# Optimization experiments

Measured on AMD Instinct MI355X. Metric: run time of the kernel, lower is better.

The kernel has to match this reference:

```python
import jax, jax.numpy as jnp
import numpy as np

B, S, D = 2, 2048, 1024
H, DH, DL, DR = 16, 64, 512, 64
DHID, N_SHARED, N_ROUTED, TOPK = 512, 2, 8, 2
EPS = 1e-6


def setup_inputs() -> dict:
    key = jax.random.key(0)
    ks = jax.random.split(key, 16)
    w = lambda k, shp: jax.random.normal(k, shp, dtype=jnp.float32) * 0.02
    return {
        "x": jax.random.normal(ks[0], (B, S, D), dtype=jnp.float32),
        "mask": jnp.tril(jnp.ones((S, S), dtype=bool)),  # causal
        "w_q": w(ks[1], (D, H * (DH + DR))),
        "w_dkv": w(ks[2], (D, DL)),
        "w_uk": w(ks[3], (DL, H * DH)),
        "w_uv": w(ks[4], (DL, H * DH)),
        "w_kr": w(ks[5], (D, DR)),
        "w_o": w(ks[6], (H * DH, D)),
        "attn_norm_w": jnp.ones((D,), jnp.float32),
        "mlp_norm_w": jnp.ones((D,), jnp.float32),
        "gate_w": w(ks[7], (D, N_ROUTED)),
        "wr_gate": w(ks[8], (N_ROUTED, D, DHID)),
        "wr_up": w(ks[9], (N_ROUTED, D, DHID)),
        "wr_down": w(ks[10], (N_ROUTED, DHID, D)),
        "ws_gate": w(ks[11], (N_SHARED, D, DHID)),
        "ws_up": w(ks[12], (N_SHARED, D, DHID)),
        "ws_down": w(ks[13], (N_SHARED, DHID, D)),
    }


def _rmsnorm(x, w):
    x32 = x.astype(jnp.float32)
    n = x32 * jax.lax.rsqrt(jnp.mean(x32 * x32, axis=-1, keepdims=True) + EPS)
    return n.astype(x.dtype) * w


def _rope_tables(seq_len, dim):
    half = dim // 2
    inv = 1.0 / (10000.0 ** (jnp.arange(half, dtype=jnp.float32) / half))
    ang = jnp.arange(seq_len, dtype=jnp.float32)[:, None] * inv[None, :]  # [S, dim/2]
    return jnp.cos(ang), jnp.sin(ang)


def _rope(t, cos, sin):
    # t: [..., S, dim]; rotate-half convention
    t1, t2 = jnp.split(t, 2, axis=-1)
    return jnp.concatenate([t1 * cos - t2 * sin, t2 * cos + t1 * sin], axis=-1)


def _layer(x, mask, w_q, w_dkv, w_uk, w_uv, w_kr, w_o, attn_norm_w, mlp_norm_w,
           gate_w, wr_gate, wr_up, wr_down, ws_gate, ws_up, ws_down):
    # ---- pre-norm MLA attention + residual ----
    h = _rmsnorm(x, attn_norm_w)
    cos, sin = _rope_tables(S, DR)

    q = (h @ w_q).reshape(B, S, H, DH + DR).transpose(0, 2, 1, 3)  # [B,H,S,DH+DR]
    q_c, q_r = q[..., :DH], _rope(q[..., DH:], cos, sin)

    latent = h @ w_dkv                                              # [B,S,DL]
    k_c = (latent @ w_uk).reshape(B, S, H, DH).transpose(0, 2, 1, 3)  # [B,H,S,DH]
    v = (latent @ w_uv).reshape(B, S, H, DH).transpose(0, 2, 1, 3)
    k_r = _rope(h @ w_kr, cos, sin)                                 # [B,S,DR] shared across heads

    scale = 1.0 / np.sqrt(DH + DR)
    scores = (jnp.einsum("bhqd,bhkd->bhqk", q_c, k_c)
              + jnp.einsum("bhqd,bkd->bhqk", q_r, k_r)) * scale
    scores = jnp.where(mask, scores, jnp.float32(-1e9))
    attn = jax.nn.softmax(scores, axis=-1)
    ctx = jnp.einsum("bhqk,bhkd->bhqd", attn, v)                    # [B,H,S,DH]
    attn_out = ctx.transpose(0, 2, 1, 3).reshape(B, S, H * DH) @ w_o
    x = x + attn_out

    # ---- pre-norm shared + routed MoE FFN + residual ----
    h = _rmsnorm(x, mlp_norm_w).reshape(-1, D)                      # [T,D]
    probs = jax.nn.softmax(h @ gate_w, axis=-1)                     # [T,NR]
    vals, idx = jax.lax.top_k(probs, TOPK)                          # [T,K]
    gw = vals / jnp.sum(vals, axis=-1, keepdims=True)
    dense_w = jnp.sum(jax.nn.one_hot(idx, N_ROUTED, dtype=h.dtype) * gw[..., None], axis=1)  # [T,NR]

    g = jax.nn.silu(jnp.einsum("td,edh->teh", h, wr_gate))
    u = jnp.einsum("td,edh->teh", h, wr_up)
    y = jnp.einsum("teh,ehd->ted", g * u, wr_down)                  # [T,NR,D]
    routed = jnp.einsum("ted,te->td", y, dense_w)

    gs = jax.nn.silu(jnp.einsum("td,sdh->tsh", h, ws_gate))
    us = jnp.einsum("td,sdh->tsh", h, ws_up)
    shared = jnp.einsum("tsh,shd->td", gs * us, ws_down)

    return x + (routed + shared).reshape(B, S, D)


def reference(x, mask, w_q, w_dkv, w_uk, w_uv, w_kr, w_o, attn_norm_w, mlp_norm_w,
              gate_w, wr_gate, wr_up, wr_down, ws_gate, ws_up, ws_down):
    return _layer(x, mask, w_q, w_dkv, w_uk, w_uv, w_kr, w_o, attn_norm_w, mlp_norm_w,
                  gate_w, wr_gate, wr_up, wr_down, ws_gate, ws_up, ws_down)
```

## Files before the change

### kernel.cpp

```cpp
#include <hip/hip_runtime.h>
#include <hip/hip_bf16.h>
#include <stdint.h>

typedef unsigned short u16;
typedef __attribute__((ext_vector_type(8))) short short8;
typedef __attribute__((ext_vector_type(4))) float f32x4;
typedef __attribute__((ext_vector_type(4))) int i32x4;
typedef __attribute__((ext_vector_type(2))) unsigned int u32x2;

#define B_    2
#define S_    2048
#define D_    1024
#define H_    16
#define T_    (B_*S_)

static __device__ __forceinline__ float b2f(u16 h) { return __uint_as_float(((uint32_t)h) << 16); }
static __device__ __forceinline__ u16 f2b(float f) {
    uint32_t u = __float_as_uint(f);
    u += 0x7fffu + ((u >> 16) & 1u);
    return (u16)(u >> 16);
}
static __device__ __forceinline__ uint32_t pack2(float a, float b) {
    return (uint32_t)f2b(a) | ((uint32_t)f2b(b) << 16);
}
static __device__ __forceinline__ uint32_t cvtpk(float a, float b) {
    uint32_t r;
    asm("v_cvt_pk_bf16_f32 %0, %1, %2" : "=v"(r) : "v"(a), "v"(b));
    return r;
}
#define MFMA(a,b,c) __builtin_amdgcn_mfma_f32_16x16x32_bf16(a,b,c,0,0,0)

static __device__ __forceinline__ void gl2lds16(const void* g, void* l) {
    __builtin_amdgcn_global_load_lds((const __attribute__((address_space(1))) void*)g,
                                     (__attribute__((address_space(3))) void*)l, 16, 0, 0);
}

__global__ __launch_bounds__(256) void transpose_cvt(const float* __restrict__ in,
    u16* __restrict__ out, int K, int N, long inEZ, long outEZ)
{
    __shared__ float tile[32][33];
    const int e = blockIdx.z;
    const float* ip = in + (long)e * inEZ;
    u16* op = out + (long)e * outEZ;
    int n0 = blockIdx.x * 32, k0 = blockIdx.y * 32;
    int tx = threadIdx.x, ty = threadIdx.y;
#pragma unroll
    for (int i = 0; i < 4; ++i) {
        int k = k0 + ty + 8 * i, n = n0 + tx;
        tile[ty + 8 * i][tx] = (k < K && n < N) ? ip[(long)k * N + n] : 0.f;
    }
    __syncthreads();
#pragma unroll
    for (int i = 0; i < 4; ++i) {
        int n = n0 + ty + 8 * i, k = k0 + tx;
        if (n < N && k < K) op[(long)n * K + k] = f2b(tile[tx][ty + 8 * i]);
    }
}

__global__ __launch_bounds__(256) void gemm_k(const u16* __restrict__ A, long lda,
    const u16* __restrict__ Bt, long ldb, void* __restrict__ Cv, long ldc, int K,
    int mode, const float* __restrict__ resid)
{
    __shared__ u16 As[128 * 32];
    __shared__ u16 Bs[128 * 32];
    const int tid = threadIdx.x, lane = tid & 63, wave = tid >> 6;
    const int wm = (wave & 1) * 64, wn = (wave >> 1) * 64;
    const int quad = lane >> 4, rr = lane & 15, q8 = quad * 8;
    const long row0 = (long)blockIdx.y * 128, col0 = (long)blockIdx.x * 128;
    f32x4 acc[4][4];
#pragma unroll
    for (int i = 0; i < 4; ++i)
#pragma unroll
        for (int j = 0; j < 4; ++j)
#pragma unroll
            for (int c = 0; c < 4; ++c) acc[i][j][c] = 0.f;
    const int band = wave * 32;
    const u16* ga = A + (row0 + band + (lane >> 2)) * lda + (lane & 3) * 8;
    const u16* gb = Bt + (col0 + band + (lane >> 2)) * ldb + (lane & 3) * 8;
    u16* la = &As[band * 32];
    u16* lb = &Bs[band * 32];
    for (int k0 = 0; k0 < K; k0 += 32) {
        gl2lds16(ga + k0, la);
        gl2lds16(ga + k0 + 16 * lda, la + 16 * 32);
        gl2lds16(gb + k0, lb);
        gl2lds16(gb + k0 + 16 * ldb, lb + 16 * 32);
        __syncthreads();
        short8 af[4], bf[4];
#pragma unroll
        for (int mi = 0; mi < 4; ++mi) af[mi] = *(const short8*)&As[(wm + mi * 16 + rr) * 32 + q8];
#pragma unroll
        for (int ni = 0; ni < 4; ++ni) bf[ni] = *(const short8*)&Bs[(wn + ni * 16 + rr) * 32 + q8];
#pragma unroll
        for (int mi = 0; mi < 4; ++mi)
#pragma unroll
            for (int ni = 0; ni < 4; ++ni)
                acc[mi][ni] = MFMA(af[mi], bf[ni], acc[mi][ni]);
        __syncthreads();
    }
#pragma unroll
    for (int mi = 0; mi < 4; ++mi)
#pragma unroll
        for (int ni = 0; ni < 4; ++ni)
#pragma unroll
            for (int rg = 0; rg < 4; ++rg) {
                long r = row0 + wm + mi * 16 + quad * 4 + rg;
                long c = col0 + wn + ni * 16 + rr;
                float v = acc[mi][ni][rg];
                if (mode == 1)      ((u16*)Cv)[r * ldc + c] = f2b(v);
                else if (mode == 2) ((float*)Cv)[r * ldc + c] += v;
                else                ((float*)Cv)[r * ldc + c] = v + resid[r * 1024 + c];
            }
}

__global__ __launch_bounds__(256) void gemm_shdown(const u16* __restrict__ A,
    const u16* __restrict__ BtBase, float* __restrict__ Cv)
{
    __shared__ u16 As[128 * 32];
    __shared__ u16 Bs[128 * 32];
    const int tid = threadIdx.x, lane = tid & 63, wave = tid >> 6;
    const int wm = (wave & 1) * 64, wn = (wave >> 1) * 64;
    const int quad = lane >> 4, rr = lane & 15, q8 = quad * 8;
    const long row0 = (long)blockIdx.y * 128, col0 = (long)blockIdx.x * 128;
    f32x4 acc[4][4];
#pragma unroll
    for (int i = 0; i < 4; ++i)
#pragma unroll
        for (int j = 0; j < 4; ++j)
#pragma unroll
            for (int c = 0; c < 4; ++c) acc[i][j][c] = 0.f;
    const int band = wave * 32;
    const long arow = row0 + band + (lane >> 2);
    const long brow = col0 + band + (lane >> 2);
    u16* la = &As[band * 32];
    u16* lb = &Bs[band * 32];
    for (int k0 = 0; k0 < 1024; k0 += 32) {
        const long aoff = (k0 < 512) ? (long)k0 : (long)(512 + k0);
        const long boff = (k0 < 512) ? (long)k0 : (long)(524288 - 512 + k0);
        const u16* ga = A + arow * 2048 + aoff + (lane & 3) * 8;
        const u16* gb = BtBase + brow * 512 + boff + (lane & 3) * 8;
        gl2lds16(ga, la);
        gl2lds16(ga + 16 * 2048, la + 16 * 32);
        gl2lds16(gb, lb);
        gl2lds16(gb + 16 * 512, lb + 16 * 32);
        __syncthreads();
        short8 af[4], bf[4];
#pragma unroll
        for (int mi = 0; mi < 4; ++mi) af[mi] = *(const short8*)&As[(wm + mi * 16 + rr) * 32 + q8];
#pragma unroll
        for (int ni = 0; ni < 4; ++ni) bf[ni] = *(const short8*)&Bs[(wn + ni * 16 + rr) * 32 + q8];
#pragma unroll
        for (int mi = 0; mi < 4; ++mi)
#pragma unroll
            for (int ni = 0; ni < 4; ++ni)
                acc[mi][ni] = MFMA(af[mi], bf[ni], acc[mi][ni]);
        __syncthreads();
    }
#pragma unroll
    for (int mi = 0; mi < 4; ++mi)
#pragma unroll
        for (int ni = 0; ni < 4; ++ni)
#pragma unroll
            for (int rg = 0; rg < 4; ++rg) {
                long r = row0 + wm + mi * 16 + quad * 4 + rg;
                long c = col0 + wn + ni * 16 + rr;
                Cv[r * 1024 + c] += acc[mi][ni][rg];
            }
}

__global__ __launch_bounds__(256) void gemm_gather(const u16* __restrict__ H2,
    const u16* __restrict__ BtAll, u16* __restrict__ C,
    const int* __restrict__ cnt, const int* __restrict__ off,
    const int* __restrict__ elist)
{
    const int e = blockIdx.z;
    const int cntE = cnt[e], offE = off[e];
    const int m0 = blockIdx.y * 128;
    if (m0 >= cntE) return;
    const u16* Bt = BtAll + (long)e * 1024 * 1024;
    __shared__ u16 As[128 * 32];
    __shared__ u16 Bs[128 * 32];
    const int tid = threadIdx.x, lane = tid & 63, wave = tid >> 6;
    const int wm = (wave & 1) * 64, wn = (wave >> 1) * 64;
    const int quad = lane >> 4, rr = lane & 15, q8 = quad * 8;
    const long col0 = (long)blockIdx.x * 128;
    f32x4 acc[4][4];
#pragma unroll
    for (int i = 0; i < 4; ++i)
#pragma unroll
        for (int j = 0; j < 4; ++j)
#pragma unroll
            for (int c = 0; c < 4; ++c) acc[i][j][c] = 0.f;
    const int band = wave * 32;
    int r0 = m0 + band + (lane >> 2);
    int r1 = r0 + 16;
    int tok0 = elist[offE + (r0 < cntE ? r0 : cntE - 1)];
    int tok1 = elist[offE + (r1 < cntE ? r1 : cntE - 1)];
    const u16* ga0 = H2 + (long)tok0 * 1024 + (lane & 3) * 8;
    const u16* ga1 = H2 + (long)tok1 * 1024 + (lane & 3) * 8;
    const u16* gb = Bt + (col0 + band + (lane >> 2)) * 1024L + (lane & 3) * 8;
    u16* la = &As[band * 32];
    u16* lb = &Bs[band * 32];
    for (int k0 = 0; k0 < 1024; k0 += 32) {
        gl2lds16(ga0 + k0, la);
        gl2lds16(ga1 + k0, la + 16 * 32);
        gl2lds16(gb + k0, lb);
        gl2lds16(gb + k0 + 16 * 1024, lb + 16 * 32);
        __syncthreads();
        short8 af[4], bf[4];
#pragma unroll
        for (int mi = 0; mi < 4; ++mi) af[mi] = *(const short8*)&As[(wm + mi * 16 + rr) * 32 + q8];
#pragma unroll
        for (int ni = 0; ni < 4; ++ni) bf[ni] = *(const short8*)&Bs[(wn + ni * 16 + rr) * 32 + q8];
#pragma unroll
        for (int mi = 0; mi < 4; ++mi)
#pragma unroll
            for (int ni = 0; ni < 4; ++ni)
                acc[mi][ni] = MFMA(af[mi], bf[ni], acc[mi][ni]);
        __syncthreads();
    }
#pragma unroll
    for (int mi = 0; mi < 4; ++mi)
#pragma unroll
        for (int ni = 0; ni < 4; ++ni)
#pragma unroll
            for (int rg = 0; rg < 4; ++rg) {
                int ml = wm + mi * 16 + quad * 4 + rg;
                long c = col0 + wn + ni * 16 + rr;
                if (m0 + ml < cntE)
                    C[(long)(offE + m0 + ml) * 1024 + c] = f2b(acc[mi][ni][rg]);
            }
}

__global__ __launch_bounds__(256) void gemm_slot(const u16* __restrict__ Act,
    const u16* __restrict__ BtAll, u16* __restrict__ rout,
    const int* __restrict__ cnt, const int* __restrict__ off)
{
    const int e = blockIdx.z;
    const int cntE = cnt[e], offE = off[e];
    const int m0 = blockIdx.y * 128;
    if (m0 >= cntE) return;
    const u16* Bt = BtAll + (long)e * 1024 * 512;
    __shared__ u16 As[128 * 32];
    __shared__ u16 Bs[128 * 32];
    const int tid = threadIdx.x, lane = tid & 63, wave = tid >> 6;
    const int wm = (wave & 1) * 64, wn = (wave >> 1) * 64;
    const int quad = lane >> 4, rr = lane & 15, q8 = quad * 8;
    const long col0 = (long)blockIdx.x * 128;
    f32x4 acc[4][4];
#pragma unroll
    for (int i = 0; i < 4; ++i)
#pragma unroll
        for (int j = 0; j < 4; ++j)
#pragma unroll
            for (int c = 0; c < 4; ++c) acc[i][j][c] = 0.f;
    const int band = wave * 32;
    int r0 = offE + m0 + band + (lane >> 2); if (r0 > 8191) r0 = 8191;
    int r1 = r0 + 16; if (r1 > 8191) r1 = 8191;
    const u16* ga0 = Act + (long)r0 * 1024 + (lane & 3) * 8;
    const u16* ga1 = Act + (long)r1 * 1024 + (lane & 3) * 8;
    const u16* gb = Bt + (col0 + band + (lane >> 2)) * 512L + (lane & 3) * 8;
    u16* la = &As[band * 32];
    u16* lb = &Bs[band * 32];
    for (int k0 = 0; k0 < 512; k0 += 32) {
        gl2lds16(ga0 + k0, la);
        gl2lds16(ga1 + k0, la + 16 * 32);
        gl2lds16(gb + k0, lb);
        gl2lds16(gb + k0 + 16 * 512, lb + 16 * 32);
        __syncthreads();
        short8 af[4], bf[4];
#pragma unroll
        for (int mi = 0; mi < 4; ++mi) af[mi] = *(const short8*)&As[(wm + mi * 16 + rr) * 32 + q8];
#pragma unroll
        for (int ni = 0; ni < 4; ++ni) bf[ni] = *(const short8*)&Bs[(wn + ni * 16 + rr) * 32 + q8];
#pragma unroll
        for (int mi = 0; mi < 4; ++mi)
#pragma unroll
            for (int ni = 0; ni < 4; ++ni)
                acc[mi][ni] = MFMA(af[mi], bf[ni], acc[mi][ni]);
        __syncthreads();
    }
#pragma unroll
    for (int mi = 0; mi < 4; ++mi)
#pragma unroll
        for (int ni = 0; ni < 4; ++ni)
#pragma unroll
            for (int rg = 0; rg < 4; ++rg) {
                int ml = wm + mi * 16 + quad * 4 + rg;
                long c = col0 + wn + ni * 16 + rr;
                if (m0 + ml < cntE)
                    rout[(long)(offE + m0 + ml) * 1024 + c] = f2b(acc[mi][ni][rg]);
            }
}

__global__ __launch_bounds__(256) void rmsnorm_wave(const float* __restrict__ x,
    const float* __restrict__ w, u16* __restrict__ out)
{
    const int t = blockIdx.x * 4 + (threadIdx.x >> 6);
    const int lane = threadIdx.x & 63;
    const float* xp = x + (size_t)t * D_;
    f32x4 v[4];
    float s = 0.f;
#pragma unroll
    for (int i = 0; i < 4; ++i) {
        v[i] = *(const f32x4*)&xp[lane * 4 + i * 256];
#pragma unroll
        for (int j = 0; j < 4; ++j) s += v[i][j] * v[i][j];
    }
#pragma unroll
    for (int o = 32; o > 0; o >>= 1) s += __shfl_xor(s, o);
    const float inv = rsqrtf(s * (1.f / D_) + 1e-6f);
    u16* op = out + (size_t)t * D_;
#pragma unroll
    for (int i = 0; i < 4; ++i) {
        const int d = lane * 4 + i * 256;
        f32x4 wv = *(const f32x4*)&w[d];
        u32x2 pk;
        pk[0] = pack2(v[i][0] * inv * wv[0], v[i][1] * inv * wv[1]);
        pk[1] = pack2(v[i][2] * inv * wv[2], v[i][3] * inv * wv[3]);
        *(u32x2*)&op[d] = pk;
    }
}

__global__ __launch_bounds__(256) void rmsnorm_gate_fused(const float* __restrict__ xm,
    const float* __restrict__ nw, const float* __restrict__ gw, u16* __restrict__ h2,
    int* __restrict__ tok_e, float* __restrict__ tok_w)
{
    const int t = blockIdx.x * 4 + (threadIdx.x >> 6);
    const int lane = threadIdx.x & 63;
    const float* xp = xm + (size_t)t * D_;
    f32x4 v[4];
    float s = 0.f;
#pragma unroll
    for (int i = 0; i < 4; ++i) {
        v[i] = *(const f32x4*)&xp[lane * 4 + i * 256];
#pragma unroll
        for (int j = 0; j < 4; ++j) s += v[i][j] * v[i][j];
    }
#pragma unroll
    for (int o = 32; o > 0; o >>= 1) s += __shfl_xor(s, o);
    const float inv = rsqrtf(s * (1.f / D_) + 1e-6f);
    u16* op = h2 + (size_t)t * D_;
    float part[8] = {0,0,0,0,0,0,0,0};
#pragma unroll
    for (int i = 0; i < 4; ++i) {
        const int d = lane * 4 + i * 256;
        f32x4 wv = *(const f32x4*)&nw[d];
        float hv[4];
#pragma unroll
        for (int j = 0; j < 4; ++j) hv[j] = v[i][j] * inv * wv[j];
        u32x2 pk;
        pk[0] = pack2(hv[0], hv[1]);
        pk[1] = pack2(hv[2], hv[3]);
        *(u32x2*)&op[d] = pk;
#pragma unroll
        for (int j = 0; j < 4; ++j) {
            const float* gp = gw + (size_t)(d + j) * 8;
#pragma unroll
            for (int e = 0; e < 8; ++e) part[e] += hv[j] * gp[e];
        }
    }
#pragma unroll
    for (int e = 0; e < 8; ++e)
#pragma unroll
        for (int o = 32; o > 0; o >>= 1) part[e] += __shfl_xor(part[e], o);
    if (lane == 0) {
        float mx = part[0];
#pragma unroll
        for (int e = 1; e < 8; ++e) mx = fmaxf(mx, part[e]);
        float p[8];
#pragma unroll
        for (int e = 0; e < 8; ++e) p[e] = __expf(part[e] - mx);
        int i0 = 0;
#pragma unroll
        for (int e = 1; e < 8; ++e) if (p[e] > p[i0]) i0 = e;
        int i1 = (i0 == 0) ? 1 : 0;
#pragma unroll
        for (int e = 0; e < 8; ++e) { if (e == i0) continue; if (p[e] > p[i1]) i1 = e; }
        float sw = p[i0] + p[i1];
        tok_e[2 * t] = i0;  tok_e[2 * t + 1] = i1;
        tok_w[2 * t] = p[i0] / sw;  tok_w[2 * t + 1] = p[i1] / sw;
    }
}

__global__ __launch_bounds__(256) void moe_route(const int* __restrict__ tok_e,
    int* __restrict__ cnt, int* __restrict__ off,
    int* __restrict__ elist, int* __restrict__ tslot)
{
    const int E = blockIdx.x;
    const int tid = threadIdx.x, lane = tid & 63, wave = tid >> 6;
    int ev[32];
#pragma unroll
    for (int i = 0; i < 8; ++i)
        *(i32x4*)&ev[i * 4] = *(const i32x4*)&tok_e[tid * 32 + i * 4];
    int c8[8] = {0,0,0,0,0,0,0,0};
#pragma unroll
    for (int k = 0; k < 32; ++k) ++c8[ev[k] & 7];
    int incl[8];
#pragma unroll
    for (int e = 0; e < 8; ++e) {
        int vv = c8[e];
#pragma unroll
        for (int d = 1; d < 64; d <<= 1) {
            int tmp = __shfl_up(vv, d);
            if (lane >= d) vv += tmp;
        }
        incl[e] = vv;
    }
    __shared__ int wtot[4][8];
    if (lane == 63)
#pragma unroll
        for (int e = 0; e < 8; ++e) wtot[wave][e] = incl[e];
    __syncthreads();
    int tot[8];
#pragma unroll
    for (int e = 0; e < 8; ++e) tot[e] = wtot[0][e] + wtot[1][e] + wtot[2][e] + wtot[3][e];
    int waveoff = 0;
    for (int w = 0; w < 4; ++w) if (w < wave) waveoff += wtot[w][E];
    int offE = 0;
#pragma unroll
    for (int e = 0; e < 8; ++e) if (e < E) offE += tot[e];
    int rank = offE + waveoff + (incl[E] - c8[E]);
#pragma unroll
    for (int k = 0; k < 32; ++k) {
        if ((ev[k] & 7) == E) {
            int p = tid * 32 + k;
            elist[rank] = p >> 1;
            tslot[p] = rank;
            ++rank;
        }
    }
    if (tid == 0) { cnt[E] = tot[E]; off[E] = offE; }
}

__global__ __launch_bounds__(256) void rope_all(u16* __restrict__ proj)
{
    int idx = blockIdx.x * 256 + threadIdx.x;
    int i = idx & 31;
    int r = idx >> 5;
    int t = r / 17, which = r - t * 17;
    int s = t & (S_ - 1);
    float inv = __expf(-(float)i * 0.28782313662425575f);
    float ang = (float)s * inv;
    float c = cosf(ang), sn = sinf(ang);
    u16* base = proj + (size_t)t * 2688 + (which < 16 ? which * 128 + 64 : 2560);
    float t1 = b2f(base[i]), t2 = b2f(base[32 + i]);
    base[i]      = f2b(t1 * c - t2 * sn);
    base[32 + i] = f2b(t2 * c + t1 * sn);
}

#define KS  136
#define PS2 72
__global__ __launch_bounds__(256, 4) void attn_flash(const u16* __restrict__ proj,
    const u16* __restrict__ kc, const u16* __restrict__ vt, u16* __restrict__ ctx)
{
    const int qidx = blockIdx.x >> 5;
    const int qt = (qidx < 16) ? (31 - qidx) : (qidx - 16);
    const int bh = blockIdx.x & 31;
    const int b = bh >> 4, h = bh & 15;
    const int q0 = qt * 64;
    const int tid = threadIdx.x, lane = tid & 63, wave = tid >> 6;
    const int quad = lane >> 4, rr = lane & 15, q8 = quad * 8;
    const int wm2 = wave * 16;

    __shared__ u16 Ks[64 * KS];
    __shared__ u16 Ps[64 * PS2];

    const long tbase = (long)b * S_ + q0;
    short8 qf[4];
#pragma unroll
    for (int d0 = 0; d0 < 4; ++d0)
        qf[d0] = *(const short8*)&proj[(tbase + wm2 + rr) * 2688 + h * 128 + d0 * 32 + q8];

    f32x4 accO[4];
    float m_i = -3e38f, l_i = 0.f;
#pragma unroll
    for (int vi = 0; vi < 4; ++vi)
#pragma unroll
        for (int rg = 0; rg < 4; ++rg) accO[vi][rg] = 0.f;
    const float sc = 0.08838834764831845f * 1.4426950408889634f;

    const int srow0 = tid >> 3, scc0 = (tid & 7) * 8;
    const u16* kcp = kc   + ((long)b * S_ + srow0) * 1024 + h * 64 + scc0;
    const u16* krp = proj + ((long)b * S_ + srow0) * 2688 + 2560 + scc0;
    const u16* vbase = vt + (size_t)(h * 64 + rr) * 4096 + b * 2048 + q8;

    const int nkt = qt + 1;
    short8 rk0 = *(const short8*)(kcp);
    short8 rk1 = *(const short8*)(kcp + 32 * 1024);
    short8 rm0 = *(const short8*)(krp);
    short8 rm1 = *(const short8*)(krp + (size_t)32 * 2688);

    for (int kt = 0; kt < nkt; ++kt) {
        const int k0 = kt * 64;
        *(short8*)&Ks[srow0 * KS + scc0]        = rk0;
        *(short8*)&Ks[(srow0 + 32) * KS + scc0] = rk1;
        *(short8*)&Ks[srow0 * KS + 64 + scc0]        = rm0;
        *(short8*)&Ks[(srow0 + 32) * KS + 64 + scc0] = rm1;
        __syncthreads();

        const size_t k0s = (kt + 1 < nkt) ? (size_t)(k0 + 64) : 0;
        short8 nk0 = *(const short8*)(kcp + k0s * 1024);
        short8 nk1 = *(const short8*)(kcp + k0s * 1024 + 32 * 1024);
        short8 nm0 = *(const short8*)(krp + k0s * 2688);
        short8 nm1 = *(const short8*)(krp + k0s * 2688 + (size_t)32 * 2688);

        f32x4 accS[4];
#pragma unroll
        for (int ki = 0; ki < 4; ++ki)
#pragma unroll
            for (int rg = 0; rg < 4; ++rg) accS[ki][rg] = 0.f;
        __builtin_amdgcn_s_setprio(1);
#pragma unroll
        for (int d0 = 0; d0 < 4; ++d0) {
            short8 kf[4];
#pragma unroll
            for (int ki = 0; ki < 4; ++ki) kf[ki] = *(const short8*)&Ks[(ki * 16 + rr) * KS + d0 * 32 + q8];
#pragma unroll
            for (int ki = 0; ki < 4; ++ki) accS[ki] = MFMA(kf[ki], qf[d0], accS[ki]);
        }
        __builtin_amdgcn_s_setprio(0);
        __syncthreads();

        short8 vf0[4], vf1[4];
#pragma unroll
        for (int vi = 0; vi < 4; ++vi) {
            vf0[vi] = *(const short8*)(vbase + (size_t)vi * 16 * 4096 + k0);
            vf1[vi] = *(const short8*)(vbase + (size_t)vi * 16 * 4096 + k0 + 32);
        }

        float mx = -3e38f;
        if (kt == qt) {
            const int qg = q0 + wm2 + rr;
#pragma unroll
            for (int ki = 0; ki < 4; ++ki)
#pragma unroll
                for (int rg = 0; rg < 4; ++rg) {
                    float w = accS[ki][rg] * sc;
                    if (k0 + ki * 16 + quad * 4 + rg > qg) w = -1e30f;
                    accS[ki][rg] = w;
                    mx = fmaxf(mx, w);
                }
        } else {
#pragma unroll
            for (int ki = 0; ki < 4; ++ki)
#pragma unroll
                for (int rg = 0; rg < 4; ++rg) {
                    float w = accS[ki][rg] * sc;
                    accS[ki][rg] = w;
                    mx = fmaxf(mx, w);
                }
        }
        mx = fmaxf(mx, __shfl_xor(mx, 16));
        mx = fmaxf(mx, __shfl_xor(mx, 32));
        if (__any(mx > m_i)) {
            float mnew = fmaxf(m_i, mx);
            float alpha = exp2f(m_i - mnew);
            m_i = mnew;
            l_i *= alpha;
#pragma unroll
            for (int vi = 0; vi < 4; ++vi)
#pragma unroll
                for (int rg = 0; rg < 4; ++rg) accO[vi][rg] *= alpha;
        }
        float ps = 0.f;
#pragma unroll
        for (int ki = 0; ki < 4; ++ki) {
            float p0 = exp2f(accS[ki][0] - m_i);
            float p1 = exp2f(accS[ki][1] - m_i);
            float p2 = exp2f(accS[ki][2] - m_i);
            float p3 = exp2f(accS[ki][3] - m_i);
            ps += (p0 + p1) + (p2 + p3);
            u32x2 pk; pk[0] = cvtpk(p0, p1); pk[1] = cvtpk(p2, p3);
            *(u32x2*)&Ps[(wm2 + rr) * PS2 + ki * 16 + quad * 4] = pk;
        }
        ps += __shfl_xor(ps, 16);
        ps += __shfl_xor(ps, 32);
        l_i += ps;

        short8 pf0 = *(const short8*)&Ps[(wm2 + rr) * PS2 + q8];
        short8 pf1 = *(const short8*)&Ps[(wm2 + rr) * PS2 + 32 + q8];
        __builtin_amdgcn_s_setprio(1);
#pragma unroll
        for (int vi = 0; vi < 4; ++vi) accO[vi] = MFMA(vf0[vi], pf0, accO[vi]);
#pragma unroll
        for (int vi = 0; vi < 4; ++vi) accO[vi] = MFMA(vf1[vi], pf1, accO[vi]);
        __builtin_amdgcn_s_setprio(0);

        rk0 = nk0; rk1 = nk1; rm0 = nm0; rm1 = nm1;
    }
    {
        float linv = 1.f / l_i;
        long t = tbase + wm2 + rr;
#pragma unroll
        for (int vi = 0; vi < 4; ++vi) {
            u32x2 pk;
            pk[0] = pack2(accO[vi][0] * linv, accO[vi][1] * linv);
            pk[1] = pack2(accO[vi][2] * linv, accO[vi][3] * linv);
            *(u32x2*)&ctx[t * 1024 + h * 64 + vi * 16 + quad * 4] = pk;
        }
    }
}

__global__ __launch_bounds__(256) void silu_mul(u16* __restrict__ gu, int nPairRows)
{
    int i = blockIdx.x * 256 + threadIdx.x;
    if (i >= nPairRows * 64) return;
    int row = i >> 6, j8 = (i & 63) * 8;
    long base = (long)row * 1024;
    short8 g8 = *(const short8*)&gu[base + j8];
    short8 u8 = *(const short8*)&gu[base + 512 + j8];
    short8 r;
#pragma unroll
    for (int j = 0; j < 8; ++j) {
        float g = b2f((u16)g8[j]), u = b2f((u16)u8[j]);
        r[j] = (short)f2b(g / (1.f + __expf(-g)) * u);
    }
    *(short8*)&gu[base + j8] = r;
}

__global__ __launch_bounds__(256) void final_kernel(const float* __restrict__ xm,
    const u16* __restrict__ rout, const int* __restrict__ tok_slot,
    const float* __restrict__ tok_w, float* __restrict__ out)
{
    long i = ((long)blockIdx.x * 256 + threadIdx.x) * 4;
    int t = (int)(i >> 10), d = (int)(i & 1023);
    int s0 = tok_slot[2 * t], s1 = tok_slot[2 * t + 1];
    float w0 = tok_w[2 * t], w1 = tok_w[2 * t + 1];
    f32x4 xv = *(const f32x4*)&xm[i];
    u32x2 r0 = *(const u32x2*)&rout[(long)s0 * 1024 + d];
    u32x2 r1 = *(const u32x2*)&rout[(long)s1 * 1024 + d];
    f32x4 o;
    o[0] = xv[0] + w0 * b2f((u16)(r0[0] & 0xffffu)) + w1 * b2f((u16)(r1[0] & 0xffffu));
    o[1] = xv[1] + w0 * b2f((u16)(r0[0] >> 16))     + w1 * b2f((u16)(r1[0] >> 16));
    o[2] = xv[2] + w0 * b2f((u16)(r0[1] & 0xffffu)) + w1 * b2f((u16)(r1[1] & 0xffffu));
    o[3] = xv[3] + w0 * b2f((u16)(r0[1] >> 16))     + w1 * b2f((u16)(r1[1] >> 16));
    *(f32x4*)&out[i] = o;
}

#define OFF_XMID   0UL
#define OFF_H      16777216UL
#define OFF_PROJ   25165824UL
#define OFF_WGU    25165824UL
#define OFF_KC     47185920UL
#define OFF_WD     47185920UL
#define OFF_VT     55574528UL
#define OFF_GUR    57671680UL
#define OFF_CTX    63963136UL
#define OFF_WATT   72351744UL
#define OFF_ROUT   74448896UL
#define OFF_GUS    91226112UL
#define OFF_TOKE   108003328UL
#define OFF_TOKW   108036096UL
#define OFF_TSLOT  108068864UL
#define OFF_ELIST  108101632UL
#define OFF_META   108134400UL

extern "C" void kernel_launch(void* const* d_in, const int* in_sizes, int n_in,
                              void* d_out, int out_size, void* d_ws, size_t ws_size,
                              hipStream_t stream)
{
    const float* x       = (const float*)d_in[0];
    const float* w_q     = (const float*)d_in[2];
    const float* w_dkv   = (const float*)d_in[3];
    const float* w_uk    = (const float*)d_in[4];
    const float* w_uv    = (const float*)d_in[5];
    const float* w_kr    = (const float*)d_in[6];
    const float* w_o     = (const float*)d_in[7];
    const float* attn_nw = (const float*)d_in[8];
    const float* mlp_nw  = (const float*)d_in[9];
    const float* gate_w  = (const float*)d_in[10];
    const float* wr_gate = (const float*)d_in[11];
    const float* wr_up   = (const float*)d_in[12];
    const float* wr_down = (const float*)d_in[13];
    const float* ws_gate = (const float*)d_in[14];
    const float* ws_up   = (const float*)d_in[15];
    const float* ws_down = (const float*)d_in[16];
    float* out = (float*)d_out;

    char* W = (char*)d_ws;
    float* x_mid = (float*)(W + OFF_XMID);
    u16* h      = (u16*)(W + OFF_H);
    u16* h2     = (u16*)(W + OFF_H);
    u16* proj   = (u16*)(W + OFF_PROJ);
    u16* wgu_t  = (u16*)(W + OFF_WGU);
    u16* kc     = (u16*)(W + OFF_KC);
    u16* wd_t   = (u16*)(W + OFF_WD);
    u16* vt     = (u16*)(W + OFF_VT);
    u16* gu_r   = (u16*)(W + OFF_GUR);
    u16* ctx    = (u16*)(W + OFF_CTX);
    u16* wqkv_t = (u16*)(W + OFF_WATT);
    u16* wuk_t  = wqkv_t + 2688 * 1024;
    u16* wuv_t  = wuk_t + 1024 * 512;
    u16* wo_t   = wuv_t + 1024 * 512;
    u16* rout   = (u16*)(W + OFF_ROUT);
    u16* gu_s   = (u16*)(W + OFF_GUS);
    int*   tok_e = (int*)(W + OFF_TOKE);
    float* tok_w = (float*)(W + OFF_TOKW);
    int*   tslot = (int*)(W + OFF_TSLOT);
    int*   elist = (int*)(W + OFF_ELIST);
    int*   meta  = (int*)(W + OFF_META);
    int* cnt = meta, * off = meta + 8;

    dim3 tb(32, 8);
    transpose_cvt<<<dim3(64, 32, 1), tb, 0, stream>>>(w_q,   wqkv_t,               1024, 2048, 0, 0);
    transpose_cvt<<<dim3(16, 32, 1), tb, 0, stream>>>(w_dkv, wqkv_t + 2048 * 1024, 1024, 512,  0, 0);
    transpose_cvt<<<dim3(2,  32, 1), tb, 0, stream>>>(w_kr,  wqkv_t + 2560 * 1024, 1024, 64,   0, 0);
    transpose_cvt<<<dim3(32, 16, 1), tb, 0, stream>>>(w_uk,  wuk_t,                512,  1024, 0, 0);
    transpose_cvt<<<dim3(32, 16, 1), tb, 0, stream>>>(w_uv,  wuv_t,                512,  1024, 0, 0);
    transpose_cvt<<<dim3(32, 32, 1), tb, 0, stream>>>(w_o,   wo_t,                 1024, 1024, 0, 0);

    rmsnorm_wave<<<T_ / 4, 256, 0, stream>>>(x, attn_nw, h);
    gemm_k<<<dim3(21, 32), 256, 0, stream>>>(h, 1024, wqkv_t, 1024, proj, 2688, 1024, 1, nullptr);
    rope_all<<<(T_ * 17 * 32) / 256, 256, 0, stream>>>(proj);
    gemm_k<<<dim3(8, 32), 256, 0, stream>>>(proj + 2048, 2688, wuk_t, 512, kc, 1024, 512, 1, nullptr);
    gemm_k<<<dim3(32, 8), 256, 0, stream>>>(wuv_t, 512, proj + 2048, 2688, vt, 4096, 512, 1, nullptr);
    attn_flash<<<1024, 256, 0, stream>>>(proj, kc, vt, ctx);
    gemm_k<<<dim3(8, 32), 256, 0, stream>>>(ctx, 1024, wo_t, 1024, x_mid, 1024, 1024, 3, x);

    transpose_cvt<<<dim3(16, 32, 8), tb, 0, stream>>>(wr_gate, wgu_t,              1024, 512, 524288, 1048576);
    transpose_cvt<<<dim3(16, 32, 8), tb, 0, stream>>>(wr_up,   wgu_t + 512 * 1024, 1024, 512, 524288, 1048576);
    transpose_cvt<<<dim3(16, 32, 2), tb, 0, stream>>>(ws_gate, wgu_t + 8 * 1048576,              1024, 512, 524288, 1048576);
    transpose_cvt<<<dim3(16, 32, 2), tb, 0, stream>>>(ws_up,   wgu_t + 8 * 1048576 + 512 * 1024, 1024, 512, 524288, 1048576);
    transpose_cvt<<<dim3(32, 16, 8), tb, 0, stream>>>(wr_down, wd_t,               512, 1024, 524288, 524288);
    transpose_cvt<<<dim3(32, 16, 2), tb, 0, stream>>>(ws_down, wd_t + 8 * 524288,  512, 1024, 524288, 524288);

    rmsnorm_gate_fused<<<T_ / 4, 256, 0, stream>>>(x_mid, mlp_nw, gate_w, h2, tok_e, tok_w);
    moe_route<<<8, 256, 0, stream>>>(tok_e, cnt, off, elist, tslot);
    gemm_gather<<<dim3(8, 64, 8), 256, 0, stream>>>(h2, wgu_t, gu_r, cnt, off, elist);
    silu_mul<<<(8192 * 64) / 256, 256, 0, stream>>>(gu_r, 8192);
    gemm_slot<<<dim3(8, 64, 8), 256, 0, stream>>>(gu_r, wd_t, rout, cnt, off);
    gemm_k<<<dim3(16, 32), 256, 0, stream>>>(h2, 1024, wgu_t + 8 * 1048576, 1024, gu_s, 2048, 1024, 1, nullptr);
    silu_mul<<<(8192 * 64) / 256, 256, 0, stream>>>(gu_s, 8192);
    gemm_shdown<<<dim3(8, 32), 256, 0, stream>>>(gu_s, wd_t + 8 * 524288, x_mid);
    final_kernel<<<(T_ * D_) / 1024, 256, 0, stream>>>(x_mid, rout, tslot, tok_w, out);
}
```

Measured before the change: 571.4 us.

## Swizzle attention LDS tiles with XOR instead of padding and reorder query tiles

Replaces the padded shared-memory layouts for the K tile and P tile in the flash-attention kernel with XOR-swizzled unpadded layouts. This shrinks LDS use and aims to avoid bank conflicts on reads and writes. It also changes the order in which query tiles are assigned to blocks, interleaving heavy and light causal tiles in two groups to balance load. The risk is that a swizzle index error corrupts results, and the attention kernel is only part of the total layer time.

```diff
diff --git a/kernel.cpp b/kernel.cpp
--- a/kernel.cpp
+++ b/kernel.cpp
@@ -448,13 +448,12 @@
     base[32 + i] = f2b(t2 * c + t1 * sn);
 }
 
-#define KS  136
-#define PS2 72
 __global__ __launch_bounds__(256, 4) void attn_flash(const u16* __restrict__ proj,
     const u16* __restrict__ kc, const u16* __restrict__ vt, u16* __restrict__ ctx)
 {
     const int qidx = blockIdx.x >> 5;
-    const int qt = (qidx < 16) ? (31 - qidx) : (qidx - 16);
+    const int qt = (qidx < 8) ? (31 - qidx) : (qidx < 16) ? (qidx - 8)
+                 : (qidx < 24) ? (39 - qidx) : (qidx - 16);
     const int bh = blockIdx.x & 31;
     const int b = bh >> 4, h = bh & 15;
     const int q0 = qt * 64;
@@ -462,8 +461,8 @@
     const int quad = lane >> 4, rr = lane & 15, q8 = quad * 8;
     const int wm2 = wave * 16;
 
-    __shared__ u16 Ks[64 * KS];
-    __shared__ u16 Ps[64 * PS2];
+    __shared__ u16 Ks[64 * 128];
+    __shared__ u16 Ps[64 * 64];
 
     const long tbase = (long)b * S_ + q0;
     short8 qf[4];
@@ -479,10 +478,18 @@
         for (int rg = 0; rg < 4; ++rg) accO[vi][rg] = 0.f;
     const float sc = 0.08838834764831845f * 1.4426950408889634f;
 
-    const int srow0 = tid >> 3, scc0 = (tid & 7) * 8;
-    const u16* kcp = kc   + ((long)b * S_ + srow0) * 1024 + h * 64 + scc0;
-    const u16* krp = proj + ((long)b * S_ + srow0) * 2688 + 2560 + scc0;
+    const int srow0 = tid >> 3, sg = tid & 7;
+    const int swz = sg ^ (srow0 & 7);
+    const u16* kcp = kc   + ((long)b * S_ + srow0) * 1024 + h * 64 + sg * 8;
+    const u16* krp = proj + ((long)b * S_ + srow0) * 2688 + 2560 + sg * 8;
     const u16* vbase = vt + (size_t)(h * 64 + rr) * 4096 + b * 2048 + q8;
+    const int rg7 = rr & 7;
+    int rdcol[4];
+#pragma unroll
+    for (int d0 = 0; d0 < 4; ++d0) rdcol[d0] = ((d0 * 4 + quad) ^ rg7) * 8;
+    const int pwcol0 = ((quad * 8) ^ (rg7 << 3));
+    const int prcol0 = (((quad * 16) ^ (rg7 << 4)) >> 1);
+    const int prcol1 = (((64 + quad * 16) ^ (rg7 << 4)) >> 1);
 
     const int nkt = qt + 1;
     short8 rk0 = *(const short8*)(kcp);
@@ -492,10 +499,10 @@
 
     for (int kt = 0; kt < nkt; ++kt) {
         const int k0 = kt * 64;
-        *(short8*)&Ks[srow0 * KS + scc0]        = rk0;
-        *(short8*)&Ks[(srow0 + 32) * KS + scc0] = rk1;
-        *(short8*)&Ks[srow0 * KS + 64 + scc0]        = rm0;
-        *(short8*)&Ks[(srow0 + 32) * KS + 64 + scc0] = rm1;
+        *(short8*)&Ks[srow0 * 128 + swz * 8]             = rk0;
+        *(short8*)&Ks[(srow0 + 32) * 128 + swz * 8]      = rk1;
+        *(short8*)&Ks[srow0 * 128 + 64 + swz * 8]        = rm0;
+        *(short8*)&Ks[(srow0 + 32) * 128 + 64 + swz * 8] = rm1;
         __syncthreads();
 
         const size_t k0s = (kt + 1 < nkt) ? (size_t)(k0 + 64) : 0;
@@ -514,7 +521,7 @@
         for (int d0 = 0; d0 < 4; ++d0) {
             short8 kf[4];
 #pragma unroll
-            for (int ki = 0; ki < 4; ++ki) kf[ki] = *(const short8*)&Ks[(ki * 16 + rr) * KS + d0 * 32 + q8];
+            for (int ki = 0; ki < 4; ++ki) kf[ki] = *(const short8*)&Ks[(ki * 16 + rr) * 128 + rdcol[d0]];
 #pragma unroll
             for (int ki = 0; ki < 4; ++ki) accS[ki] = MFMA(kf[ki], qf[d0], accS[ki]);
         }
@@ -571,14 +578,14 @@
             float p3 = exp2f(accS[ki][3] - m_i);
             ps += (p0 + p1) + (p2 + p3);
             u32x2 pk; pk[0] = cvtpk(p0, p1); pk[1] = cvtpk(p2, p3);
-            *(u32x2*)&Ps[(wm2 + rr) * PS2 + ki * 16 + quad * 4] = pk;
+            *(u32x2*)&Ps[(wm2 + rr) * 64 + ((((ki * 32 + quad * 8) ^ (rg7 << 4)) >> 1))] = pk;
         }
         ps += __shfl_xor(ps, 16);
         ps += __shfl_xor(ps, 32);
         l_i += ps;
 
-        short8 pf0 = *(const short8*)&Ps[(wm2 + rr) * PS2 + q8];
-        short8 pf1 = *(const short8*)&Ps[(wm2 + rr) * PS2 + 32 + q8];
+        short8 pf0 = *(const short8*)&Ps[(wm2 + rr) * 64 + prcol0];
+        short8 pf1 = *(const short8*)&Ps[(wm2 + rr) * 64 + prcol1];
         __builtin_amdgcn_s_setprio(1);
 #pragma unroll
         for (int vi = 0; vi < 4; ++vi) accO[vi] = MFMA(vf0[vi], pf0, accO[vi]);
@@ -599,6 +606,7 @@
             *(u32x2*)&ctx[t * 1024 + h * 64 + vi * 16 + quad * 4] = pk;
         }
     }
+    (void)pwcol0;
 }
 
 __global__ __launch_bounds__(256) void silu_mul(u16* __restrict__ gu, int nPairRows)
```

Measured after the change: 580.8 us. No clear change (+1.7%).
